# Kernel tuning notes

Measured on AMD Instinct MI355X. Metric: run time of the kernel, lower is better.

The kernel has to match this reference:

```python
import jax, jax.numpy as jnp
import numpy as np

B, S, L = 2, 2048, 2048
H, KVH, D = 16, 4, 128
HID = H * D
EPS = 1e-6
SCALE = 1.0 / np.sqrt(D)


def rmsnorm(x, w, eps=EPS):
    # normalize over last dim (head_size), fp32 math
    xf = x.astype(jnp.float32)
    var = jnp.mean(xf * xf, axis=-1, keepdims=True)
    return (xf * jax.lax.rsqrt(var + eps)).astype(x.dtype) * w


def setup_inputs() -> dict:
    key = jax.random.key(0)
    ks = jax.random.split(key, 5)
    s = 1.0 / np.sqrt(HID)
    return {
        "x": jax.random.normal(ks[0], (B, S, HID), jnp.float32),
        "c": jax.random.normal(ks[1], (B, L, HID), jnp.float32),
        "wq": jax.random.normal(ks[2], (HID, H * D), jnp.float32) * s,
        "wkv": jax.random.normal(ks[3], (HID, KVH * D * 2), jnp.float32) * s,
        "wo": jax.random.normal(ks[4], (H * D, HID), jnp.float32) * s,
        "norm_q_w": jnp.ones((D,), jnp.float32),
        "norm_k_w": jnp.ones((D,), jnp.float32),
    }


def reference(x, c, wq, wkv, wo, norm_q_w, norm_k_w):
    bs, seq_len, _ = x.shape
    c_len = c.shape[1]
    n_rep = H // KVH
    # Q projection + per-head RMSNorm
    xq = (x @ wq).reshape(bs, seq_len, H, D)
    xq = rmsnorm(xq, norm_q_w)
    # packed KV projection: view(..., kvh, hd, 2), unbind last dim
    ckv = (c @ wkv).reshape(bs, c_len, KVH, D, 2)
    ck, cv = ckv[..., 0], ckv[..., 1]
    ck = rmsnorm(ck, norm_k_w)
    # GQA repeat_kv (repeat_interleave over head dim)
    ck = jnp.repeat(ck, n_rep, axis=2)  # [b, L, H, D]
    cv = jnp.repeat(cv, n_rep, axis=2)
    # SDPA cross-attention, softmax in fp32
    scores = jnp.einsum("bqhd,bkhd->bhqk", xq, ck) * SCALE
    attn = jax.nn.softmax(scores.astype(jnp.float32), axis=-1).astype(xq.dtype)
    out = jnp.einsum("bhqk,bkhd->bqhd", attn, cv)
    out = out.reshape(bs, seq_len, H * D)
    return out @ wo
```

## Files before the change

### kernel.cpp

```cpp
#include <hip/hip_runtime.h>

#define B_ 2
#define S_ 2048
#define L_ 2048
#define H_ 16
#define KVH_ 4
#define D_ 128
#define HID_ 2048
#define EPS_ 1e-6f

typedef unsigned short u16;
typedef unsigned int u32;
typedef __bf16 bf16x8 __attribute__((ext_vector_type(8)));
typedef float f32x4 __attribute__((ext_vector_type(4)));
typedef unsigned u32x2v __attribute__((ext_vector_type(2)));
typedef unsigned u32x4v __attribute__((ext_vector_type(4)));

__device__ __forceinline__ float bf2f(u32 u) {
  union { u32 i; float f; } x; x.i = u << 16; return x.f;
}
__device__ __forceinline__ u16 f2bf(float f) {
  union { float f; u32 i; } x; x.f = f;
  return (u16)((x.i + 0x7fffu + ((x.i >> 16) & 1u)) >> 16);
}
__device__ __forceinline__ u32 pack_bf16(float a, float b) {
#if __has_builtin(__builtin_amdgcn_cvt_pk_bf16_f32)
  typedef __bf16 bf16x2 __attribute__((ext_vector_type(2)));
  union { bf16x2 v; u32 u; } c;
  c.v = __builtin_amdgcn_cvt_pk_bf16_f32(a, b);
  return c.u;
#else
  return (u32)f2bf(a) | ((u32)f2bf(b) << 16);
#endif
}
__device__ __forceinline__ float fexp2(float x) {
#if __has_builtin(__builtin_amdgcn_exp2f)
  return __builtin_amdgcn_exp2f(x);
#else
  return exp2f(x);
#endif
}
__device__ __forceinline__ void gl2lds16(const u16* g, u16* l) {
  __builtin_amdgcn_global_load_lds(
      (const __attribute__((address_space(1))) u32*)g,
      (__attribute__((address_space(3))) u32*)l, 16, 0, 0);
}

#if __has_builtin(__builtin_amdgcn_permlane32_swap) && __has_builtin(__builtin_amdgcn_permlane16_swap)
#define HAS_PLS 1
#else
#define HAS_PLS 0
#endif

__device__ __forceinline__ u32x4v ctoa(u32 xa, u32 xb, u32 ya, u32 yb,
                                       int quad, int l15) {
  u32x4v f;
#if HAS_PLS
  u32x2v t1 = __builtin_amdgcn_permlane32_swap(xa, ya, false, false);
  u32x2v t2 = __builtin_amdgcn_permlane16_swap(t1.x, t1.y, false, false);
  u32x2v t3 = __builtin_amdgcn_permlane32_swap(xb, yb, false, false);
  u32x2v t4 = __builtin_amdgcn_permlane16_swap(t3.x, t3.y, false, false);
  f.x = t2.x; f.y = t4.x; f.z = t2.y; f.w = t4.y;
#else
  int a0 = (((2 * quad) & 3) * 16 + l15) << 2;
  int a1 = (((2 * quad + 1) & 3) * 16 + l15) << 2;
  u32 xa0 = __builtin_amdgcn_ds_bpermute(a0, xa), ya0 = __builtin_amdgcn_ds_bpermute(a0, ya);
  u32 xb0 = __builtin_amdgcn_ds_bpermute(a0, xb), yb0 = __builtin_amdgcn_ds_bpermute(a0, yb);
  u32 xa1 = __builtin_amdgcn_ds_bpermute(a1, xa), ya1 = __builtin_amdgcn_ds_bpermute(a1, ya);
  u32 xb1 = __builtin_amdgcn_ds_bpermute(a1, xb), yb1 = __builtin_amdgcn_ds_bpermute(a1, yb);
  bool hi = quad >= 2;
  f.x = hi ? ya0 : xa0; f.y = hi ? yb0 : xb0;
  f.z = hi ? ya1 : xa1; f.w = hi ? yb1 : xb1;
#endif
  return f;
}

__global__ __launch_bounds__(256) void cvt_bf16(const float* __restrict__ in,
                                                u16* __restrict__ out, int n4) {
  int i = blockIdx.x * 256 + threadIdx.x;
  if (i >= n4) return;
  float4 v = ((const float4*)in)[i];
  uint2 o;
  o.x = pack_bf16(v.x, v.y);
  o.y = pack_bf16(v.z, v.w);
  ((uint2*)out)[i] = o;
}

__global__ __launch_bounds__(256) void transp_bf16(const float* __restrict__ A,
                                                   u16* __restrict__ At, int R, int C) {
  __shared__ float t[64][65];
  int c0 = blockIdx.x * 64, r0 = blockIdx.y * 64;
  int tx = threadIdx.x & 63, ty = threadIdx.x >> 6;
  for (int i = ty; i < 64; i += 4)
    t[i][tx] = A[(size_t)(r0 + i) * C + c0 + tx];
  __syncthreads();
  for (int i = ty; i < 64; i += 4)
    At[(size_t)(c0 + i) * R + r0 + tx] = f2bf(t[tx][i]);
}

__device__ __forceinline__ void store_out(u16* p, float v) { *p = f2bf(v); }
__device__ __forceinline__ void store_out(float* p, float v) { *p = v; }

template <typename OutT>
__global__ __launch_bounds__(256, 2) void gemm_bt(const u16* __restrict__ A,
                                                  const u16* __restrict__ Bt,
                                                  OutT* __restrict__ C,
                                                  int M, int N, int K) {
  __shared__ u16 sA[128 * 32];
  __shared__ u16 sB[128 * 32];
  const int tid = threadIdx.x;
  const int wave = tid >> 6, lane = tid & 63;
  const int quad = lane >> 4, l15 = lane & 15;
  const int m0 = blockIdx.x * 128, n0 = blockIdx.y * 128;
  const int wm = (wave >> 1) * 64, wn = (wave & 1) * 64;
  const u16* aP = A + (size_t)m0 * K;
  const u16* bP = Bt + (size_t)n0 * K;
  const int sr = lane >> 2;
  const int sc = (lane & 3) * 8;
  const int r0 = wave * 32, r1 = wave * 32 + 16;

  f32x4 acc[4][4];
  for (int i = 0; i < 4; i++)
    for (int j = 0; j < 4; j++)
      for (int r = 0; r < 4; r++) acc[i][j][r] = 0.0f;

  for (int k0 = 0; k0 < K; k0 += 32) {
    gl2lds16(aP + (size_t)(r0 + sr) * K + k0 + sc, &sA[r0 * 32]);
    gl2lds16(aP + (size_t)(r1 + sr) * K + k0 + sc, &sA[r1 * 32]);
    gl2lds16(bP + (size_t)(r0 + sr) * K + k0 + sc, &sB[r0 * 32]);
    gl2lds16(bP + (size_t)(r1 + sr) * K + k0 + sc, &sB[r1 * 32]);
    __syncthreads();
    bf16x8 afrag[4], bfrag[4];
    for (int i = 0; i < 4; i++)
      afrag[i] = *(const bf16x8*)&sA[(wm + i * 16 + l15) * 32 + quad * 8];
    for (int j = 0; j < 4; j++)
      bfrag[j] = *(const bf16x8*)&sB[(wn + j * 16 + l15) * 32 + quad * 8];
    for (int i = 0; i < 4; i++)
      for (int j = 0; j < 4; j++)
        acc[i][j] = __builtin_amdgcn_mfma_f32_16x16x32_bf16(afrag[i], bfrag[j], acc[i][j], 0, 0, 0);
    __syncthreads();
  }
  for (int i = 0; i < 4; i++)
    for (int j = 0; j < 4; j++) {
      int row = m0 + wm + i * 16 + quad * 4;
      int col = n0 + wn + j * 16 + l15;
      for (int r = 0; r < 4; r++)
        store_out(&C[(size_t)(row + r) * N + col], acc[i][j][r]);
    }
}

__global__ __launch_bounds__(256) void knorm_deint(const u16* __restrict__ CKV,
                                                   const float* __restrict__ w,
                                                   u16* __restrict__ K,
                                                   u16* __restrict__ Vt) {
  __shared__ u16 vbuf[128][66];
  const int tid = threadIdx.x, wave = tid >> 6, lane = tid & 63;
  const int l0 = blockIdx.x * 64, kvh = blockIdx.y, b = blockIdx.z;
  for (int it = 0; it < 16; it++) {
    int ll = wave * 16 + it;
    int row = b * L_ + l0 + ll;
    const u16* src = CKV + (size_t)row * 1024 + kvh * 256;
    u32 p0 = *(const u32*)&src[lane * 2];
    u32 p1 = *(const u32*)&src[(lane + 64) * 2];
    float k0 = bf2f(p0 & 0xffff), v0 = bf2f(p0 >> 16);
    float k1 = bf2f(p1 & 0xffff), v1 = bf2f(p1 >> 16);
    float ss = k0 * k0 + k1 * k1;
    for (int off = 1; off < 64; off <<= 1) ss += __shfl_xor(ss, off);
    float sc = rsqrtf(ss * (1.0f / 128.0f) + EPS_);
    size_t kb = (((size_t)b * KVH_ + kvh) * L_ + l0 + ll) * D_;
    K[kb + lane] = f2bf(k0 * sc * w[lane]);
    K[kb + lane + 64] = f2bf(k1 * sc * w[lane + 64]);
    vbuf[lane][ll] = f2bf(v0);
    vbuf[lane + 64][ll] = f2bf(v1);
  }
  __syncthreads();
  for (int it = tid; it < 128 * 32; it += 256) {
    int d = it >> 5, cc = (it & 31) * 2;
    u32 pk = (u32)vbuf[d][cc] | ((u32)vbuf[d][cc + 1] << 16);
    *(u32*)&Vt[(((size_t)b * KVH_ + kvh) * D_ + d) * L_ + l0 + cc] = pk;
  }
}

__global__ __launch_bounds__(512, 4) void attn(const u16* __restrict__ XQ,
                                               const float* __restrict__ nw,
                                               const u16* __restrict__ K,
                                               const u16* __restrict__ Vt,
                                               u16* __restrict__ AO) {
  __shared__ u16 sk[2][4][64 * 32];
  __shared__ u16 sv[2][2][128 * 32];
  const int tid = threadIdx.x, wave = tid >> 6, lane = tid & 63;
  const int quad = lane >> 4, l15 = lane & 15;
  const int qt = blockIdx.x, h = blockIdx.y, b = blockIdx.z;
  const int kvh = h >> 2;
  const int s0 = qt * 128, wr0 = wave * 16;

  const u16* kbase = K + ((size_t)(b * KVH_ + kvh) * L_) * D_;
  const u16* vbase = Vt + ((size_t)(b * KVH_ + kvh) * D_) * L_;
  const int srow = lane >> 2;
  const int scol = ((lane & 3) ^ ((lane >> 3) & 3)) * 8;
  const int swq = (quad ^ ((l15 >> 1) & 3)) * 8;
  const int kch = wave >> 1, khalf = wave & 1;
  const int vch = wave >> 2, vqtr = wave & 3;

  auto stage = [&](int l0, int buf) {
    const u16* kb = kbase + (size_t)l0 * D_ + kch * 32;
    for (int is = 0; is < 2; is++) {
      int row = khalf * 32 + is * 16;
      gl2lds16(kb + (size_t)(row + srow) * D_ + scol, &sk[buf][kch][row * 32]);
    }
    const u16* vb = vbase + l0 + vch * 32;
    for (int is = 0; is < 2; is++) {
      int drow = vqtr * 32 + is * 16;
      gl2lds16(vb + (size_t)(drow + srow) * L_ + scol, &sv[buf][vch][drow * 32]);
    }
  };

  bf16x8 qf[4];
  {
    const float cexp = 0.12753102331322172f;
    const u16* qr = XQ + (size_t)(b * S_ + s0 + wr0 + l15) * HID_ + h * D_;
    float vals[4][8];
    float ss = 0.0f;
    for (int kc = 0; kc < 4; kc++) {
      uint4 u = *(const uint4*)&qr[kc * 32 + quad * 8];
      u32 uu[4] = {u.x, u.y, u.z, u.w};
      for (int e = 0; e < 4; e++) {
        float lo = bf2f(uu[e] & 0xffff), hi = bf2f(uu[e] >> 16);
        vals[kc][2 * e] = lo;
        vals[kc][2 * e + 1] = hi;
        ss += lo * lo + hi * hi;
      }
    }
    ss += __shfl_xor(ss, 16);
    ss += __shfl_xor(ss, 32);
    float scale = rsqrtf(ss * (1.0f / 128.0f) + EPS_) * cexp;
    for (int kc = 0; kc < 4; kc++) {
      float4 w0 = *(const float4*)&nw[kc * 32 + quad * 8];
      float4 w1 = *(const float4*)&nw[kc * 32 + quad * 8 + 4];
      union { u32x4v u; bf16x8 v; } q;
      q.u.x = pack_bf16(vals[kc][0] * scale * w0.x, vals[kc][1] * scale * w0.y);
      q.u.y = pack_bf16(vals[kc][2] * scale * w0.z, vals[kc][3] * scale * w0.w);
      q.u.z = pack_bf16(vals[kc][4] * scale * w1.x, vals[kc][5] * scale * w1.y);
      q.u.w = pack_bf16(vals[kc][6] * scale * w1.z, vals[kc][7] * scale * w1.w);
      qf[kc] = q.v;
    }
  }

  float psum = 0.0f;
  f32x4 o[8];
  for (int n = 0; n < 8; n++)
    for (int r = 0; r < 4; r++) o[n][r] = 0.0f;

  stage(0, 0);
  int cur = 0;
  const int NT = L_ / 64;
  for (int t = 0; t < NT; t++) {
    if (t + 1 < NT) {
      stage((t + 1) * 64, cur ^ 1);
      asm volatile("s_waitcnt vmcnt(4)\n\ts_barrier" ::: "memory");
    } else {
      asm volatile("s_waitcnt vmcnt(0)\n\ts_barrier" ::: "memory");
    }

    for (int cc = 0; cc < 2; cc++) {
      f32x4 sacc[2];
      for (int jj = 0; jj < 2; jj++)
        for (int r = 0; r < 4; r++) sacc[jj][r] = 0.0f;
      __builtin_amdgcn_s_setprio(1);
      for (int jj = 0; jj < 2; jj++) {
        int j = cc * 2 + jj;
        for (int kc = 0; kc < 4; kc++) {
          bf16x8 kf = *(const bf16x8*)&sk[cur][kc][(j * 16 + l15) * 32 + swq];
          sacc[jj] = __builtin_amdgcn_mfma_f32_16x16x32_bf16(kf, qf[kc], sacc[jj], 0, 0, 0);
        }
      }
      __builtin_amdgcn_s_setprio(0);
      union { u32x4v u; bf16x8 v; } pf;
      {
        float p0[4], p1[4];
        for (int r = 0; r < 4; r++) {
          p0[r] = fexp2(sacc[0][r]);
          p1[r] = fexp2(sacc[1][r]);
          psum += p0[r] + p1[r];
        }
        u32 xa = pack_bf16(p0[0], p0[1]), xb = pack_bf16(p0[2], p0[3]);
        u32 ya = pack_bf16(p1[0], p1[1]), yb = pack_bf16(p1[2], p1[3]);
        pf.u = ctoa(xa, xb, ya, yb, quad, l15);
      }
      __builtin_amdgcn_s_setprio(1);
      for (int n = 0; n < 8; n++) {
        bf16x8 vf = *(const bf16x8*)&sv[cur][cc][(n * 16 + l15) * 32 + swq];
        o[n] = __builtin_amdgcn_mfma_f32_16x16x32_bf16(pf.v, vf, o[n], 0, 0, 0);
      }
      __builtin_amdgcn_s_setprio(0);
    }
    asm volatile("s_barrier" ::: "memory");
    cur ^= 1;
  }

  {
    float s = psum;
    s += __shfl_xor(s, 16);
    s += __shfl_xor(s, 32);
    float linv = 1.0f / s;
    float lr[4];
    for (int r = 0; r < 4; r++) lr[r] = __shfl(linv, quad * 4 + r);
    u16* ob = AO + (size_t)(b * S_ + s0 + wr0) * HID_ + h * D_;
    for (int n = 0; n < 8; n++)
      for (int r = 0; r < 4; r++)
        ob[(size_t)(quad * 4 + r) * HID_ + n * 16 + l15] = f2bf(o[n][r] * lr[r]);
  }
}

extern "C" void kernel_launch(void* const* d_in, const int* in_sizes, int n_in,
                              void* d_out, int out_size, void* d_ws, size_t ws_size,
                              hipStream_t stream) {
  const float* x = (const float*)d_in[0];
  const float* c = (const float*)d_in[1];
  const float* wq = (const float*)d_in[2];
  const float* wkv = (const float*)d_in[3];
  const float* wo = (const float*)d_in[4];
  const float* nqw = (const float*)d_in[5];
  const float* nkw = (const float*)d_in[6];
  float* out = (float*)d_out;

  const int M = B_ * S_;
  char* p = (char*)d_ws;
  auto alloc = [&](size_t bytes) {
    char* r = p;
    p += (bytes + 255) & ~(size_t)255;
    return r;
  };
  u16* xbf = (u16*)alloc((size_t)M * HID_ * 2);
  u16* cbf = (u16*)alloc((size_t)M * HID_ * 2);
  u16* wqT = (u16*)alloc((size_t)HID_ * HID_ * 2);
  u16* wkvT = (u16*)alloc((size_t)1024 * HID_ * 2);
  u16* woT = (u16*)alloc((size_t)HID_ * HID_ * 2);
  u16* XQ = (u16*)alloc((size_t)M * HID_ * 2);
  u16* CKV = (u16*)alloc((size_t)M * 1024 * 2);
  u16* Kb = (u16*)alloc((size_t)B_ * KVH_ * L_ * D_ * 2);
  u16* Vt = (u16*)alloc((size_t)B_ * KVH_ * D_ * L_ * 2);
  u16* AO = (u16*)alloc((size_t)M * HID_ * 2);

  cvt_bf16<<<8192, 256, 0, stream>>>(x, xbf, M * HID_ / 4);
  cvt_bf16<<<8192, 256, 0, stream>>>(c, cbf, M * HID_ / 4);
  transp_bf16<<<dim3(32, 32), 256, 0, stream>>>(wq, wqT, HID_, HID_);
  transp_bf16<<<dim3(16, 32), 256, 0, stream>>>(wkv, wkvT, HID_, 1024);
  transp_bf16<<<dim3(32, 32), 256, 0, stream>>>(wo, woT, HID_, HID_);
  gemm_bt<u16><<<dim3(32, 16), 256, 0, stream>>>(xbf, wqT, XQ, M, HID_, HID_);
  gemm_bt<u16><<<dim3(32, 8), 256, 0, stream>>>(cbf, wkvT, CKV, M, 1024, HID_);
  knorm_deint<<<dim3(32, 4, 2), 256, 0, stream>>>(CKV, nkw, Kb, Vt);
  attn<<<dim3(16, 16, 2), 512, 0, stream>>>(XQ, nqw, Kb, Vt, AO);
  gemm_bt<float><<<dim3(32, 16), 256, 0, stream>>>(AO, woT, out, M, HID_, HID_);
}
```

Before: 383.4 us.

## Split attention key range across wave halves and merge partial outputs in LDS

The attention block now covers 64 query rows instead of 128. The two wave groups each handle one half of every 64-key tile, and their partial outputs and row sums are combined through shared memory at the end. This doubles the grid to 1024 blocks so the GPU has more parallelism and is better filled, and it halves per-wave serial work per tile. In exchange, each K/V tile is loaded by twice as many blocks, and there is an extra LDS reduction plus a barrier in the epilogue.

```diff
diff --git a/kernel.cpp b/kernel.cpp
--- a/kernel.cpp
+++ b/kernel.cpp
@@ -186,13 +186,16 @@
                                                const u16* __restrict__ K,
                                                const u16* __restrict__ Vt,
                                                u16* __restrict__ AO) {
-  __shared__ u16 sk[2][4][64 * 32];
-  __shared__ u16 sv[2][2][128 * 32];
+  __shared__ union __align__(16) SMem {
+    struct { u16 sk[2][4][64 * 32]; u16 sv[2][2][128 * 32]; } s;
+    struct { float ob[4][16][132]; float ps[4][16]; } e;
+  } sm;
   const int tid = threadIdx.x, wave = tid >> 6, lane = tid & 63;
   const int quad = lane >> 4, l15 = lane & 15;
   const int qt = blockIdx.x, h = blockIdx.y, b = blockIdx.z;
   const int kvh = h >> 2;
-  const int s0 = qt * 128, wr0 = wave * 16;
+  const int qsub = wave & 3, lh = wave >> 2;
+  const int s0 = qt * 64, wr0 = qsub * 16;
 
   const u16* kbase = K + ((size_t)(b * KVH_ + kvh) * L_) * D_;
   const u16* vbase = Vt + ((size_t)(b * KVH_ + kvh) * D_) * L_;
@@ -206,12 +209,12 @@
     const u16* kb = kbase + (size_t)l0 * D_ + kch * 32;
     for (int is = 0; is < 2; is++) {
       int row = khalf * 32 + is * 16;
-      gl2lds16(kb + (size_t)(row + srow) * D_ + scol, &sk[buf][kch][row * 32]);
+      gl2lds16(kb + (size_t)(row + srow) * D_ + scol, &sm.s.sk[buf][kch][row * 32]);
     }
     const u16* vb = vbase + l0 + vch * 32;
     for (int is = 0; is < 2; is++) {
       int drow = vqtr * 32 + is * 16;
-      gl2lds16(vb + (size_t)(drow + srow) * L_ + scol, &sv[buf][vch][drow * 32]);
+      gl2lds16(vb + (size_t)(drow + srow) * L_ + scol, &sm.s.sv[buf][vch][drow * 32]);
     }
   };
 
@@ -262,15 +265,15 @@
       asm volatile("s_waitcnt vmcnt(0)\n\ts_barrier" ::: "memory");
     }
 
-    for (int cc = 0; cc < 2; cc++) {
+    {
       f32x4 sacc[2];
       for (int jj = 0; jj < 2; jj++)
         for (int r = 0; r < 4; r++) sacc[jj][r] = 0.0f;
       __builtin_amdgcn_s_setprio(1);
       for (int jj = 0; jj < 2; jj++) {
-        int j = cc * 2 + jj;
+        int j = lh * 2 + jj;
         for (int kc = 0; kc < 4; kc++) {
-          bf16x8 kf = *(const bf16x8*)&sk[cur][kc][(j * 16 + l15) * 32 + swq];
+          bf16x8 kf = *(const bf16x8*)&sm.s.sk[cur][kc][(j * 16 + l15) * 32 + swq];
           sacc[jj] = __builtin_amdgcn_mfma_f32_16x16x32_bf16(kf, qf[kc], sacc[jj], 0, 0, 0);
         }
       }
@@ -289,7 +292,7 @@
       }
       __builtin_amdgcn_s_setprio(1);
       for (int n = 0; n < 8; n++) {
-        bf16x8 vf = *(const bf16x8*)&sv[cur][cc][(n * 16 + l15) * 32 + swq];
+        bf16x8 vf = *(const bf16x8*)&sm.s.sv[cur][lh][(n * 16 + l15) * 32 + swq];
         o[n] = __builtin_amdgcn_mfma_f32_16x16x32_bf16(pf.v, vf, o[n], 0, 0, 0);
       }
       __builtin_amdgcn_s_setprio(0);
@@ -298,17 +301,27 @@
     cur ^= 1;
   }
 
-  {
-    float s = psum;
-    s += __shfl_xor(s, 16);
-    s += __shfl_xor(s, 32);
-    float linv = 1.0f / s;
+  float sred = psum;
+  sred += __shfl_xor(sred, 16);
+  sred += __shfl_xor(sred, 32);
+  if (lh == 1) {
+    for (int n = 0; n < 8; n++)
+      for (int r = 0; r < 4; r++)
+        sm.e.ob[qsub][quad * 4 + r][n * 16 + l15] = o[n][r];
+    if (quad == 0) sm.e.ps[qsub][l15] = sred;
+  }
+  __syncthreads();
+  if (lh == 0) {
+    float stot = sred + sm.e.ps[qsub][l15];
+    float linv = 1.0f / stot;
     float lr[4];
     for (int r = 0; r < 4; r++) lr[r] = __shfl(linv, quad * 4 + r);
     u16* ob = AO + (size_t)(b * S_ + s0 + wr0) * HID_ + h * D_;
     for (int n = 0; n < 8; n++)
-      for (int r = 0; r < 4; r++)
-        ob[(size_t)(quad * 4 + r) * HID_ + n * 16 + l15] = f2bf(o[n][r] * lr[r]);
+      for (int r = 0; r < 4; r++) {
+        float v = o[n][r] + sm.e.ob[qsub][quad * 4 + r][n * 16 + l15];
+        ob[(size_t)(quad * 4 + r) * HID_ + n * 16 + l15] = f2bf(v * lr[r]);
+      }
   }
 }
 
@@ -350,6 +363,6 @@
   gemm_bt<u16><<<dim3(32, 16), 256, 0, stream>>>(xbf, wqT, XQ, M, HID_, HID_);
   gemm_bt<u16><<<dim3(32, 8), 256, 0, stream>>>(cbf, wkvT, CKV, M, 1024, HID_);
   knorm_deint<<<dim3(32, 4, 2), 256, 0, stream>>>(CKV, nkw, Kb, Vt);
-  attn<<<dim3(16, 16, 2), 512, 0, stream>>>(XQ, nqw, Kb, Vt, AO);
+  attn<<<dim3(32, 16, 2), 512, 0, stream>>>(XQ, nqw, Kb, Vt, AO);
   gemm_bt<float><<<dim3(32, 16), 256, 0, stream>>>(AO, woT, out, M, HID_, HID_);
 }
```

After: 403.4 us. 1.05x slower.
